# Optimization experiments

Hardware: AMD Instinct MI355X
Metric: run time of the kernel (lower is better)

The kernel has to match this reference:

```python
import jax, jax.numpy as jnp
import numpy as np

H = 16  # num_attention_heads


def setup_inputs() -> dict:
    key = jax.random.key(0)
    k1, k2, k3 = jax.random.split(key, 3)
    B, S, E = 2, 2048, 1024
    return {
        "hidden_states": jax.random.normal(k1, (B, S, E), dtype=jnp.float32),
        "W_attn": jax.random.normal(k2, (E, 3 * E), dtype=jnp.float32) * 0.02,
        "b_attn": jnp.zeros((3 * E,), dtype=jnp.float32),
        "W_proj": jax.random.normal(k3, (E, E), dtype=jnp.float32) * 0.02,
        "b_proj": jnp.zeros((E,), dtype=jnp.float32),
    }


def reference(hidden_states, W_attn, b_attn, W_proj, b_proj):
    B, S, E = hidden_states.shape
    hd = E // H
    # Conv1D: x @ W + b -> [B, S, 3E]
    qkv = hidden_states @ W_attn + b_attn
    # Faithful to module: _split_heads with 3*head_dim FIRST, then split q/k/v.
    # i.e. per-head slice of size 3*hd is [q_h | k_h | v_h] (interleaved layout).
    qkv = qkv.reshape(B, S, H, 3 * hd).transpose(0, 2, 1, 3)  # [B, H, S, 3*hd]
    q, k, v = jnp.split(qkv, 3, axis=-1)                      # each [B, H, S, hd]
    # scores, scaled by sqrt(head_dim) (value.size(-1) ** 0.5)
    scores = jnp.einsum("bhqd,bhkd->bhqk", q, k) / jnp.asarray(hd, q.dtype) ** 0.5
    # causal mask via where with masked_bias = -10000.0 (not -inf), as in module
    causal = jnp.tril(jnp.ones((S, S), dtype=bool))
    scores = jnp.where(causal, scores, jnp.asarray(-10000.0, scores.dtype))
    attn_weights = jax.nn.softmax(scores, axis=-1)  # dropout p=0 -> identity
    attn_out = jnp.einsum("bhqk,bhkd->bhqd", attn_weights, v)
    attn_out = attn_out.transpose(0, 2, 1, 3).reshape(B, S, E)  # merge heads
    return attn_out @ W_proj + b_proj
```

## Files before the change

### kernel.cpp

```cpp
#include <hip/hip_runtime.h>
#include <hip/hip_bf16.h>


typedef __attribute__((ext_vector_type(4))) float f32x4;
typedef __attribute__((ext_vector_type(8))) short short8;

#define AS1 __attribute__((address_space(1)))
#define AS3 __attribute__((address_space(3)))

__device__ __forceinline__ void load_lds16(const void* g, void* l) {
    __builtin_amdgcn_global_load_lds((const AS1 void*)g, (AS3 void*)l, 16, 0, 0);
}

__device__ __forceinline__ unsigned short f2bf(float f) {
    union { float f; unsigned int u; } v; v.f = f;
    unsigned int r = v.u + 0x7FFFu + ((v.u >> 16) & 1u);
    return (unsigned short)(r >> 16);
}

template <int CTRL>
__device__ __forceinline__ float rot_add(float x) {
    int r = __builtin_amdgcn_update_dpp(0, __builtin_bit_cast(int, x), CTRL, 0xF, 0xF, false);
    return x + __builtin_bit_cast(float, r);
}

__global__ __launch_bounds__(256) void cast_f32_bf16(
    const float* __restrict__ in, unsigned short* __restrict__ out, int n) {
    int i = (blockIdx.x * 256 + threadIdx.x) * 4;
    if (i >= n) return;
    float4 v = *(const float4*)(in + i);
    ushort4 o;
    o.x = f2bf(v.x); o.y = f2bf(v.y); o.z = f2bf(v.z); o.w = f2bf(v.w);
    *(ushort4*)(out + i) = o;
}

__global__ __launch_bounds__(256) void transpose_w(
    const float* __restrict__ W, unsigned short* __restrict__ Wt, int K, int N) {
    __shared__ float tile[32][33];
    int k0 = blockIdx.y * 32, n0 = blockIdx.x * 32;
    int t = threadIdx.x;
    int r = t >> 3, c = (t & 7) * 4;
    float4 v = *(const float4*)&W[(size_t)(k0 + r) * N + n0 + c];
    tile[r][c] = v.x; tile[r][c + 1] = v.y; tile[r][c + 2] = v.z; tile[r][c + 3] = v.w;
    __syncthreads();
    int n = t >> 3; int kk = (t & 7) * 4;
    ushort4 o;
    o.x = f2bf(tile[kk + 0][n]);
    o.y = f2bf(tile[kk + 1][n]);
    o.z = f2bf(tile[kk + 2][n]);
    o.w = f2bf(tile[kk + 3][n]);
    *(ushort4*)&Wt[(size_t)(n0 + n) * K + k0 + kk] = o;
}

template <int MODE>
__global__ __launch_bounds__(256) void gemm128(
    const unsigned short* __restrict__ A,
    const unsigned short* __restrict__ Bt,
    const float* __restrict__ bias,
    void* __restrict__ C, unsigned short* __restrict__ Vt,
    int M, int N, int K) {
    __shared__ unsigned short As[128 * 32];
    __shared__ unsigned short Bs[128 * 32];
    const int t = threadIdx.x, wave = t >> 6, lane = t & 63;
    const int l15 = lane & 15, quad = lane >> 4;
    const int m0 = blockIdx.y * 128, n0 = blockIdx.x * 128;
    const int srow = wave * 32 + (lane >> 2);
    const int sch = (lane & 3) * 8;
    const unsigned short* Ag = A + (size_t)(m0 + srow) * K + sch;
    const unsigned short* Bg = Bt + (size_t)(n0 + srow) * K + sch;
    unsigned short* AsW = &As[wave * 32 * 32];
    unsigned short* BsW = &Bs[wave * 32 * 32];
    const int wm = (wave >> 1) * 64, wn = (wave & 1) * 64;
    f32x4 acc[4][4] = {};
    for (int k0 = 0; k0 < K; k0 += 32) {
        load_lds16(Ag + k0, AsW);
        load_lds16(Ag + k0 + (size_t)16 * K, AsW + 16 * 32);
        load_lds16(Bg + k0, BsW);
        load_lds16(Bg + k0 + (size_t)16 * K, BsW + 16 * 32);
        __syncthreads();
        short8 af[4], bf[4];
#pragma unroll
        for (int i = 0; i < 4; ++i) {
            af[i] = *(const short8*)&As[(wm + i * 16 + l15) * 32 + quad * 8];
            bf[i] = *(const short8*)&Bs[(wn + i * 16 + l15) * 32 + quad * 8];
        }
#pragma unroll
        for (int mt = 0; mt < 4; ++mt)
#pragma unroll
            for (int nt = 0; nt < 4; ++nt)
                acc[mt][nt] = __builtin_amdgcn_mfma_f32_16x16x32_bf16(af[mt], bf[nt], acc[mt][nt], 0, 0, 0);
        __syncthreads();
    }
#pragma unroll
    for (int mt = 0; mt < 4; ++mt) {
        int mrow = m0 + wm + mt * 16 + quad * 4;
#pragma unroll
        for (int nt = 0; nt < 4; ++nt) {
            int col = n0 + wn + nt * 16 + l15;
            float bv = bias[col];
            if (MODE == 0) {
                float* Cf = (float*)C;
#pragma unroll
                for (int r = 0; r < 4; ++r)
                    Cf[(size_t)(mrow + r) * N + col] = acc[mt][nt][r] + bv;
            } else {
                int h = col / 192;
                int j = col - h * 192;
                if (j < 128) {
                    unsigned short* qkp = (unsigned short*)C;
#pragma unroll
                    for (int r = 0; r < 4; ++r)
                        qkp[(size_t)(mrow + r) * 2048 + h * 128 + j] = f2bf(acc[mt][nt][r] + bv);
                } else {
                    int b = mrow >> 11, s0 = mrow & 2047;
                    int d = j - 128;
                    ushort4 pk;
                    pk.x = f2bf(acc[mt][nt][0] + bv);
                    pk.y = f2bf(acc[mt][nt][1] + bv);
                    pk.z = f2bf(acc[mt][nt][2] + bv);
                    pk.w = f2bf(acc[mt][nt][3] + bv);
                    *(ushort4*)&Vt[((size_t)(b * 16 + h) * 64 + d) * 2048 + s0] = pk;
                }
            }
        }
    }
}

__device__ __forceinline__ void attn_tile(
    f32x4 (&o)[4], float (&lrun)[4],
    const short8 (&qf)[2],
    const unsigned short (*Ks)[72], const unsigned short (*Vts)[72],
    unsigned short (*Psw)[72],
    bool diag, int wave, int l15, int quad) {
    f32x4 s[4] = {};
#pragma unroll
    for (int km = 0; km < 2; ++km)
#pragma unroll
        for (int nt = 0; nt < 4; ++nt) {
            short8 kf = *(const short8*)&Ks[nt * 16 + l15][km * 32 + quad * 8];
            s[nt] = __builtin_amdgcn_mfma_f32_16x16x32_bf16(qf[km], kf, s[nt], 0, 0, 0);
        }
    float lt[4] = {0.f, 0.f, 0.f, 0.f};
#pragma unroll
    for (int nt = 0; nt < 4; ++nt)
#pragma unroll
        for (int r = 0; r < 4; ++r) {
            float v = s[nt][r] * 0.125f;
            if (diag && (nt * 16 + l15 > wave * 16 + quad * 4 + r)) v = -10000.0f;
            float pv = __expf(v);
            lt[r] += pv;
            Psw[quad * 4 + r][nt * 16 + l15] = f2bf(pv);
        }
#pragma unroll
    for (int r = 0; r < 4; ++r) {
        float v = lt[r];
        v = rot_add<0x121>(v); v = rot_add<0x122>(v);
        v = rot_add<0x124>(v); v = rot_add<0x128>(v);
        lrun[r] += v;
    }
#pragma unroll
    for (int km = 0; km < 2; ++km) {
        short8 pf = *(const short8*)&Psw[l15][km * 32 + quad * 8];
#pragma unroll
        for (int nt = 0; nt < 4; ++nt) {
            short8 vf = *(const short8*)&Vts[nt * 16 + l15][km * 32 + quad * 8];
            o[nt] = __builtin_amdgcn_mfma_f32_16x16x32_bf16(pf, vf, o[nt], 0, 0, 0);
        }
    }
}

__global__ __launch_bounds__(256) void attn1(
    const unsigned short* __restrict__ qk,
    const unsigned short* __restrict__ Vt,
    unsigned short* __restrict__ out) {
    const int S = 2048;
    __shared__ unsigned short Ks[64][72];
    __shared__ unsigned short Vts[64][72];
    __shared__ unsigned short Ps[4][16][72];
    int t = threadIdx.x, wave = t >> 6, lane = t & 63;
    int l15 = lane & 15, quad = lane >> 4;
    int bid = blockIdx.x;
    int qt = 31 - (bid >> 5);
    int bh = bid & 31;
    int b = bh >> 4, h = bh & 15;
    const unsigned short* qkb = qk + (size_t)b * S * 2048 + h * 128;
    const unsigned short* vtb = Vt + (size_t)bh * 64 * 2048;

    short8 qf[2];
    {
        int qr = qt * 64 + wave * 16 + l15;
#pragma unroll
        for (int km = 0; km < 2; ++km)
            qf[km] = *(const short8*)(qkb + (size_t)qr * 2048 + km * 32 + quad * 8);
    }
    f32x4 o[4] = {};
    float lrun[4] = {0.f, 0.f, 0.f, 0.f};

    int srow8 = t >> 3, chunk8 = (t & 7) * 8;
    int vd = t >> 2, vch = (t & 3) * 8;

    uint4 kreg0, kreg1, vreg0, vreg1;
    {
        kreg0 = *(const uint4*)(qkb + (size_t)(srow8) * 2048 + 64 + chunk8);
        kreg1 = *(const uint4*)(qkb + (size_t)(32 + srow8) * 2048 + 64 + chunk8);
        const unsigned short* vsrc = vtb + (size_t)vd * 2048;
        vreg0 = *(const uint4*)(vsrc + vch);
        vreg1 = *(const uint4*)(vsrc + vch + 32);
    }

    for (int kt = 0; kt <= qt; ++kt) {
        __syncthreads();
        *(uint4*)&Ks[srow8][chunk8] = kreg0;
        *(uint4*)&Ks[32 + srow8][chunk8] = kreg1;
        *(uint4*)&Vts[vd][vch] = vreg0;
        *(uint4*)&Vts[vd][vch + 32] = vreg1;
        __syncthreads();
        if (kt < qt) {
            int kn = kt + 1;
            kreg0 = *(const uint4*)(qkb + (size_t)(kn * 64 + srow8) * 2048 + 64 + chunk8);
            kreg1 = *(const uint4*)(qkb + (size_t)(kn * 64 + 32 + srow8) * 2048 + 64 + chunk8);
            const unsigned short* vsrc = vtb + (size_t)vd * 2048 + kn * 64;
            vreg0 = *(const uint4*)(vsrc + vch);
            vreg1 = *(const uint4*)(vsrc + vch + 32);
        }
        attn_tile(o, lrun, qf, Ks, Vts, Ps[wave], kt == qt, wave, l15, quad);
    }
    unsigned short* ob = out + (size_t)b * S * 1024 + h * 64;
#pragma unroll
    for (int r = 0; r < 4; ++r) {
        float inv = 1.0f / lrun[r];
        int srow = qt * 64 + wave * 16 + quad * 4 + r;
#pragma unroll
        for (int nt = 0; nt < 4; ++nt)
            ob[(size_t)srow * 1024 + nt * 16 + l15] = f2bf(o[nt][r] * inv);
    }
}

extern "C" void kernel_launch(void* const* d_in, const int* in_sizes, int n_in,
                              void* d_out, int out_size, void* d_ws, size_t ws_size,
                              hipStream_t stream) {
    const float* hs     = (const float*)d_in[0];
    const float* W_attn = (const float*)d_in[1];
    const float* b_attn = (const float*)d_in[2];
    const float* W_proj = (const float*)d_in[3];
    const float* b_proj = (const float*)d_in[4];
    float* out = (float*)d_out;

    const int B = 2, S = 2048, E = 1024;
    const int M = B * S;
    const int N3 = 3 * E;

    unsigned short* Xb  = (unsigned short*)d_ws;
    unsigned short* WaT = Xb + (size_t)M * E;
    unsigned short* WpT = WaT + (size_t)N3 * E;
    unsigned short* qkb = WpT + (size_t)E * E;
    unsigned short* Vt  = qkb + (size_t)M * 2048;
    unsigned short* ao  = Vt + (size_t)M * E;

    cast_f32_bf16<<<(M * E) / 1024, 256, 0, stream>>>(hs, Xb, M * E);
    transpose_w<<<dim3(N3 / 32, E / 32), 256, 0, stream>>>(W_attn, WaT, E, N3);
    transpose_w<<<dim3(E / 32, E / 32), 256, 0, stream>>>(W_proj, WpT, E, E);

    gemm128<1><<<dim3(N3 / 128, M / 128), 256, 0, stream>>>(Xb, WaT, b_attn, qkb, Vt, M, N3, E);

    attn1<<<dim3(32 * 32), 256, 0, stream>>>(qkb, Vt, ao);

    gemm128<0><<<dim3(E / 128, M / 128), 256, 0, stream>>>(ao, WpT, b_proj, out, nullptr, M, E, E);
}
```

Before: 199.1 us.

## Fuse prep kernels, stage V transpose through LDS, narrow proj GEMM tiles

Merges the activation cast and both weight transposes into one prep launch, which removes two kernel launches. The QKV GEMM now writes the V part into a shared-memory tile and stores it transposed with coalesced 16-byte rows, replacing the scattered 8-byte writes. The output projection GEMM uses 128x64 tiles so more blocks are launched on a grid that was small. The cost is an extra barrier and LDS reuse in the QKV epilogue, and less reuse of each loaded tile in the projection GEMM.

```diff
diff --git a/kernel.cpp b/kernel.cpp
--- a/kernel.cpp
+++ b/kernel.cpp
@@ -24,21 +24,11 @@
     return x + __builtin_bit_cast(float, r);
 }
 
-__global__ __launch_bounds__(256) void cast_f32_bf16(
-    const float* __restrict__ in, unsigned short* __restrict__ out, int n) {
-    int i = (blockIdx.x * 256 + threadIdx.x) * 4;
-    if (i >= n) return;
-    float4 v = *(const float4*)(in + i);
-    ushort4 o;
-    o.x = f2bf(v.x); o.y = f2bf(v.y); o.z = f2bf(v.z); o.w = f2bf(v.w);
-    *(ushort4*)(out + i) = o;
-}
-
-__global__ __launch_bounds__(256) void transpose_w(
-    const float* __restrict__ W, unsigned short* __restrict__ Wt, int K, int N) {
+__device__ __forceinline__ void transpose_tile(
+    const float* __restrict__ W, unsigned short* __restrict__ Wt,
+    int K, int N, int bx, int by, int t) {
     __shared__ float tile[32][33];
-    int k0 = blockIdx.y * 32, n0 = blockIdx.x * 32;
-    int t = threadIdx.x;
+    int k0 = by * 32, n0 = bx * 32;
     int r = t >> 3, c = (t & 7) * 4;
     float4 v = *(const float4*)&W[(size_t)(k0 + r) * N + n0 + c];
     tile[r][c] = v.x; tile[r][c + 1] = v.y; tile[r][c + 2] = v.z; tile[r][c + 3] = v.w;
@@ -52,15 +42,36 @@
     *(ushort4*)&Wt[(size_t)(n0 + n) * K + k0 + kk] = o;
 }
 
-template <int MODE>
-__global__ __launch_bounds__(256) void gemm128(
+__global__ __launch_bounds__(256) void prep(
+    const float* __restrict__ hs, unsigned short* __restrict__ Xb,
+    const float* __restrict__ W_attn, unsigned short* __restrict__ WaT,
+    const float* __restrict__ W_proj, unsigned short* __restrict__ WpT) {
+    int bid = blockIdx.x, t = threadIdx.x;
+    if (bid < 4096) {
+        int i = (bid * 256 + t) * 4;
+        float4 v = *(const float4*)(hs + i);
+        ushort4 o;
+        o.x = f2bf(v.x); o.y = f2bf(v.y); o.z = f2bf(v.z); o.w = f2bf(v.w);
+        *(ushort4*)(Xb + i) = o;
+    } else if (bid < 7168) {
+        int r = bid - 4096;
+        transpose_tile(W_attn, WaT, 1024, 3072, r % 96, r / 96, t);
+    } else {
+        int r = bid - 7168;
+        transpose_tile(W_proj, WpT, 1024, 1024, r % 32, r / 32, t);
+    }
+}
+
+__global__ __launch_bounds__(256) void gemm_qkv(
     const unsigned short* __restrict__ A,
     const unsigned short* __restrict__ Bt,
     const float* __restrict__ bias,
-    void* __restrict__ C, unsigned short* __restrict__ Vt,
+    unsigned short* __restrict__ qk, unsigned short* __restrict__ Vt,
     int M, int N, int K) {
-    __shared__ unsigned short As[128 * 32];
-    __shared__ unsigned short Bs[128 * 32];
+    __shared__ unsigned short Sh[8704];
+    unsigned short* As = Sh;
+    unsigned short* Bs = Sh + 4096;
+    unsigned short* Tb = Sh;
     const int t = threadIdx.x, wave = t >> 6, lane = t & 63;
     const int l15 = lane & 15, quad = lane >> 4;
     const int m0 = blockIdx.y * 128, n0 = blockIdx.x * 128;
@@ -91,6 +102,7 @@
                 acc[mt][nt] = __builtin_amdgcn_mfma_f32_16x16x32_bf16(af[mt], bf[nt], acc[mt][nt], 0, 0, 0);
         __syncthreads();
     }
+    const int rem = n0 % 192;
 #pragma unroll
     for (int mt = 0; mt < 4; ++mt) {
         int mrow = m0 + wm + mt * 16 + quad * 4;
@@ -98,30 +110,86 @@
         for (int nt = 0; nt < 4; ++nt) {
             int col = n0 + wn + nt * 16 + l15;
             float bv = bias[col];
-            if (MODE == 0) {
-                float* Cf = (float*)C;
+            int h = col / 192;
+            int j = col - h * 192;
+            if (j < 128) {
 #pragma unroll
                 for (int r = 0; r < 4; ++r)
-                    Cf[(size_t)(mrow + r) * N + col] = acc[mt][nt][r] + bv;
+                    qk[(size_t)(mrow + r) * 2048 + h * 128 + j] = f2bf(acc[mt][nt][r] + bv);
             } else {
-                int h = col / 192;
-                int j = col - h * 192;
-                if (j < 128) {
-                    unsigned short* qkp = (unsigned short*)C;
-#pragma unroll
-                    for (int r = 0; r < 4; ++r)
-                        qkp[(size_t)(mrow + r) * 2048 + h * 128 + j] = f2bf(acc[mt][nt][r] + bv);
-                } else {
-                    int b = mrow >> 11, s0 = mrow & 2047;
-                    int d = j - 128;
-                    ushort4 pk;
-                    pk.x = f2bf(acc[mt][nt][0] + bv);
-                    pk.y = f2bf(acc[mt][nt][1] + bv);
-                    pk.z = f2bf(acc[mt][nt][2] + bv);
-                    pk.w = f2bf(acc[mt][nt][3] + bv);
-                    *(ushort4*)&Vt[((size_t)(b * 16 + h) * 64 + d) * 2048 + s0] = pk;
-                }
+                int d = j - 128;
+                int s_local = wm + mt * 16 + quad * 4;
+                ushort4 pk;
+                pk.x = f2bf(acc[mt][nt][0] + bv);
+                pk.y = f2bf(acc[mt][nt][1] + bv);
+                pk.z = f2bf(acc[mt][nt][2] + bv);
+                pk.w = f2bf(acc[mt][nt][3] + bv);
+                *(ushort4*)&Tb[d * 136 + s_local] = pk;
             }
+        }
+    }
+    if (rem != 0) {
+        __syncthreads();
+        int vhalf = (rem == 64) ? 1 : 0;
+        int h = (n0 + vhalf * 64) / 192;
+        int b = m0 >> 11;
+        unsigned short* vbase = Vt + ((size_t)(b * 16 + h) * 64) * 2048 + (m0 & 2047);
+        int drow = t >> 4, ch = (t & 15) * 8;
+#pragma unroll
+        for (int rr = 0; rr < 4; ++rr) {
+            int d = rr * 16 + drow;
+            *(uint4*)(vbase + (size_t)d * 2048 + ch) = *(const uint4*)&Tb[d * 136 + ch];
+        }
+    }
+}
+
+__global__ __launch_bounds__(256) void gemm_proj(
+    const unsigned short* __restrict__ A,
+    const unsigned short* __restrict__ Bt,
+    const float* __restrict__ bias,
+    float* __restrict__ C, int M, int N, int K) {
+    __shared__ unsigned short As[128 * 32];
+    __shared__ unsigned short Bs[64 * 32];
+    const int t = threadIdx.x, wave = t >> 6, lane = t & 63;
+    const int l15 = lane & 15, quad = lane >> 4;
+    const int m0 = blockIdx.y * 128, n0 = blockIdx.x * 64;
+    const int srowA = wave * 32 + (lane >> 2);
+    const int sch = (lane & 3) * 8;
+    const unsigned short* Ag = A + (size_t)(m0 + srowA) * K + sch;
+    const unsigned short* Bg = Bt + (size_t)(n0 + wave * 16 + (lane >> 2)) * K + sch;
+    unsigned short* AsW = &As[wave * 32 * 32];
+    unsigned short* BsW = &Bs[wave * 16 * 32];
+    const int wm = (wave >> 1) * 64, wn = (wave & 1) * 32;
+    f32x4 acc[4][2] = {};
+    for (int k0 = 0; k0 < K; k0 += 32) {
+        load_lds16(Ag + k0, AsW);
+        load_lds16(Ag + k0 + (size_t)16 * K, AsW + 16 * 32);
+        load_lds16(Bg + k0, BsW);
+        __syncthreads();
+        short8 af[4], bf[2];
+#pragma unroll
+        for (int i = 0; i < 4; ++i)
+            af[i] = *(const short8*)&As[(wm + i * 16 + l15) * 32 + quad * 8];
+#pragma unroll
+        for (int i = 0; i < 2; ++i)
+            bf[i] = *(const short8*)&Bs[(wn + i * 16 + l15) * 32 + quad * 8];
+#pragma unroll
+        for (int mt = 0; mt < 4; ++mt)
+#pragma unroll
+            for (int nt = 0; nt < 2; ++nt)
+                acc[mt][nt] = __builtin_amdgcn_mfma_f32_16x16x32_bf16(af[mt], bf[nt], acc[mt][nt], 0, 0, 0);
+        __syncthreads();
+    }
+#pragma unroll
+    for (int mt = 0; mt < 4; ++mt) {
+        int mrow = m0 + wm + mt * 16 + quad * 4;
+#pragma unroll
+        for (int nt = 0; nt < 2; ++nt) {
+            int col = n0 + wn + nt * 16 + l15;
+            float bv = bias[col];
+#pragma unroll
+            for (int r = 0; r < 4; ++r)
+                C[(size_t)(mrow + r) * N + col] = acc[mt][nt][r] + bv;
         }
     }
 }
@@ -257,13 +325,11 @@
     unsigned short* Vt  = qkb + (size_t)M * 2048;
     unsigned short* ao  = Vt + (size_t)M * E;
 
-    cast_f32_bf16<<<(M * E) / 1024, 256, 0, stream>>>(hs, Xb, M * E);
-    transpose_w<<<dim3(N3 / 32, E / 32), 256, 0, stream>>>(W_attn, WaT, E, N3);
-    transpose_w<<<dim3(E / 32, E / 32), 256, 0, stream>>>(W_proj, WpT, E, E);
-
-    gemm128<1><<<dim3(N3 / 128, M / 128), 256, 0, stream>>>(Xb, WaT, b_attn, qkb, Vt, M, N3, E);
+    prep<<<dim3(8192), 256, 0, stream>>>(hs, Xb, W_attn, WaT, W_proj, WpT);
+
+    gemm_qkv<<<dim3(N3 / 128, M / 128), 256, 0, stream>>>(Xb, WaT, b_attn, qkb, Vt, M, N3, E);
 
     attn1<<<dim3(32 * 32), 256, 0, stream>>>(qkb, Vt, ao);
 
-    gemm128<0><<<dim3(E / 128, M / 128), 256, 0, stream>>>(ao, WpT, b_proj, out, nullptr, M, E, E);
-}
+    gemm_proj<<<dim3(E / 64, M / 128), 256, 0, stream>>>(ao, WpT, b_proj, out, M, E, E);
+}
```

Result: faster. 189.6 us (-4.7%).
